# Performance work log

Hardware: AMD Instinct MI355X
Metric: run time of the kernel (lower is better)

The kernel has to match this reference:

```python
import jax, jax.numpy as jnp
import numpy as np

D_K = 256.0  # K_dim from __init__, used only as 1/sqrt(d_k) scale


def setup_inputs() -> dict:
    key = jax.random.key(0)
    ks = jax.random.split(key, 8)
    B, S, L, DQ, DK, DV, H = 8, 4096, 64, 1024, 1024, 1024, 256
    Q = jax.random.normal(ks[0], (B, S, DQ), dtype=jnp.float32)
    K = jax.random.normal(ks[1], (L, DK), dtype=jnp.float32)
    V = jax.random.normal(ks[2], (B, S, DV), dtype=jnp.float32)
    attn_mask = jax.random.randint(ks[3], (B, S, 1), 0, 2).astype(jnp.bool_)
    Wq_w = jax.random.normal(ks[4], (H, DQ), dtype=jnp.float32) * 0.02
    Wq_b = jnp.zeros((H,), dtype=jnp.float32)
    Wk_w = jax.random.normal(ks[5], (H, DK), dtype=jnp.float32) * 0.02
    Wk_b = jnp.zeros((H,), dtype=jnp.float32)
    return {"Q": Q, "K": K, "V": V, "attn_mask": attn_mask,
            "Wq_w": Wq_w, "Wq_b": Wq_b, "Wk_w": Wk_w, "Wk_b": Wk_b}


def reference(Q, K, V, attn_mask, Wq_w, Wq_b, Wk_w, Wk_b):
    # Projections (the original's expand/repeat + mul + sum is exactly a GEMM)
    kh = K @ Wk_w.T + Wk_b                                  # (L, 256)
    qh = (Q @ Wq_w.T + Wq_b) / jnp.sqrt(jnp.float32(D_K))   # (B, S, 256)
    # S[b,s,l] = sum_d qh[b,s,d]*kh[l,d]; scores sums over labels too
    S = jnp.einsum('bsd,ld->bsl', qh, kh)                   # (B, S, L)
    scores = S.sum(-1)[..., None] + attn_mask.astype(jnp.float32) * (-1e9)  # (B,S,1)
    scores = jnp.swapaxes(scores, -1, -2)                   # (B, 1, S)
    attn = jax.nn.softmax(scores, axis=-1)                  # (B, 1, S)
    context = jnp.matmul(attn, V)[:, 0, :]                  # (B, DV)
    return context, attn
```

## Files before the change

### kernel.cpp

```cpp
#include <hip/hip_runtime.h>
#include <hip/hip_bf16.h>
#include <cstddef>


#define B 8
#define S 4096
#define DQ 1024
#define H 256
#define L 64
#define RPB 16
#define NSC (S / RPB)

__global__ __launch_bounds__(256) void pre1_kernel(
        const float* __restrict__ K, const float* __restrict__ Wk_w,
        const float* __restrict__ Wk_b, float* __restrict__ ksum,
        float* __restrict__ denom) {
    __shared__ float sv[DQ];
    int t = threadIdx.x;
    if (blockIdx.x == 0 && t < B) denom[t] = 0.f;
    float4 a = {0.f, 0.f, 0.f, 0.f};
    const float* kp = K + t * 4;
#pragma unroll 8
    for (int l = 0; l < L; ++l) {
        float4 k = *(const float4*)(kp + (size_t)l * DQ);
        a.x += k.x; a.y += k.y; a.z += k.z; a.w += k.w;
    }
    *(float4*)(sv + t * 4) = a;
    __syncthreads();
    int wave = t >> 6, lane = t & 63;
    int d = blockIdx.x * 4 + wave;
    const float* wr = Wk_w + (size_t)d * DQ;
    float acc = 0.f;
#pragma unroll
    for (int j = 0; j < 4; ++j) {
        int idx = j * 256 + lane * 4;
        float4 x = *(const float4*)(wr + idx);
        float4 y = *(const float4*)(sv + idx);
        acc += x.x * y.x + x.y * y.y + x.z * y.z + x.w * y.w;
    }
    for (int off = 32; off; off >>= 1) acc += __shfl_down(acc, off);
    if (lane == 0) ksum[d] = acc + 64.f * Wk_b[d];
}

__global__ __launch_bounds__(256) void pre2_kernel(
        const float* __restrict__ Wq_w, const float* __restrict__ Wq_b,
        const float* __restrict__ ksum, float* __restrict__ w,
        float* __restrict__ bias) {
    __shared__ float ks[H];
    __shared__ float red[4][64];
    __shared__ float red2[4];
    ks[threadIdx.x] = ksum[threadIdx.x];
    __syncthreads();
    int wave = threadIdx.x >> 6, lane = threadIdx.x & 63;
    if (blockIdx.x < 16) {
        int c = blockIdx.x * 64 + lane;
        float acc = 0.f;
#pragma unroll 8
        for (int j = 0; j < 64; ++j) {
            int d = wave + 4 * j;
            acc += Wq_w[(size_t)d * DQ + c] * ks[d];
        }
        red[wave][lane] = acc;
        __syncthreads();
        if (wave == 0)
            w[c] = (red[0][lane] + red[1][lane] + red[2][lane] + red[3][lane]) * 0.0625f;
    } else {
        float v = Wq_b[threadIdx.x] * ks[threadIdx.x];
        for (int off = 32; off; off >>= 1) v += __shfl_down(v, off);
        if (lane == 0) red2[wave] = v;
        __syncthreads();
        if (threadIdx.x == 0)
            bias[0] = (red2[0] + red2[1] + red2[2] + red2[3]) * 0.0625f;
    }
}

__global__ __launch_bounds__(256) void fused_main_kernel(
        const float* __restrict__ Q, const float* __restrict__ V,
        const float* __restrict__ w, const float* __restrict__ bias,
        const int* __restrict__ mask,
        float* __restrict__ escore, float* __restrict__ denom,
        float* __restrict__ partial) {
    int sc = blockIdx.x, b = blockIdx.y, t = threadIdx.x;
    __shared__ float sp[RPB * 256];
    __shared__ float es[RPB];
    size_t rowbase = (size_t)b * S + (size_t)sc * RPB;

    const float* qb = Q + rowbase * DQ + t * 4;
    float4 wv = *(const float4*)(w + t * 4);
    float4 qv[RPB];
#pragma unroll
    for (int r = 0; r < RPB; ++r) qv[r] = *(const float4*)(qb + (size_t)r * DQ);
#pragma unroll
    for (int r = 0; r < RPB; ++r)
        sp[r * 256 + t] = qv[r].x * wv.x + qv[r].y * wv.y + qv[r].z * wv.z + qv[r].w * wv.w;
    __syncthreads();

    int r = t >> 4, j = t & 15;
    float s = 0.f;
#pragma unroll
    for (int k = 0; k < 16; ++k) s += sp[r * 256 + k * 16 + j];
    s += __shfl_xor(s, 8, 64);
    s += __shfl_xor(s, 4, 64);
    s += __shfl_xor(s, 2, 64);
    s += __shfl_xor(s, 1, 64);
    if (j == 0) {
        size_t row = rowbase + r;
        float e = mask[row] ? 0.f : __expf(s + bias[0]);
        es[r] = e;
        escore[row] = e;
    }
    __syncthreads();
    if (t == 0) {
        float d0 = 0.f;
#pragma unroll
        for (int k = 0; k < RPB; ++k) d0 += es[k];
        atomicAdd(denom + b, d0);
    }

    const float* vb = V + rowbase * DQ + t * 4;
    float4 acc = {0.f, 0.f, 0.f, 0.f};
#pragma unroll
    for (int s0 = 0; s0 < RPB; s0 += 8) {
        float4 v[8];
#pragma unroll
        for (int k = 0; k < 8; ++k) v[k] = *(const float4*)(vb + (size_t)(s0 + k) * DQ);
#pragma unroll
        for (int k = 0; k < 8; ++k) {
            float a = es[s0 + k];
            acc.x += a * v[k].x; acc.y += a * v[k].y;
            acc.z += a * v[k].z; acc.w += a * v[k].w;
        }
    }
    *(float4*)(partial + ((size_t)b * NSC + sc) * DQ + t * 4) = acc;
}

__global__ __launch_bounds__(256) void epilogue_kernel(
        const float* __restrict__ escore, const float* __restrict__ partial,
        const float* __restrict__ denom,
        float* __restrict__ ctx, float* __restrict__ attn) {
    if (blockIdx.x < 128) {
        int i = blockIdx.x * 256 + threadIdx.x;
        attn[i] = escore[i] / denom[i >> 12];
    } else {
        int idx = (blockIdx.x - 128) * 256 + threadIdx.x;
        int b = idx >> 10, d = idx & 1023;
        const float* p = partial + (size_t)b * NSC * DQ + d;
        float acc = 0.f;
#pragma unroll 8
        for (int sc = 0; sc < NSC; ++sc) acc += p[(size_t)sc * DQ];
        ctx[idx] = acc / denom[b];
    }
}

extern "C" void kernel_launch(void* const* d_in, const int* in_sizes, int n_in,
                              void* d_out, int out_size, void* d_ws, size_t ws_size,
                              hipStream_t stream) {
    const float* Q    = (const float*)d_in[0];
    const float* K    = (const float*)d_in[1];
    const float* V    = (const float*)d_in[2];
    const int*   mask = (const int*)d_in[3];
    const float* Wq_w = (const float*)d_in[4];
    const float* Wq_b = (const float*)d_in[5];
    const float* Wk_w = (const float*)d_in[6];
    const float* Wk_b = (const float*)d_in[7];

    float* ws     = (float*)d_ws;
    float* ksum   = ws;
    float* wv     = ws + 256;
    float* bias   = ws + 1280;
    float* denom  = ws + 1288;
    float* escore = ws + 4096;
    float* partial = ws + 4096 + B * S;

    float* ctx  = (float*)d_out;
    float* attn = (float*)d_out + B * DQ;

    pre1_kernel<<<H / 4, 256, 0, stream>>>(K, Wk_w, Wk_b, ksum, denom);
    pre2_kernel<<<17, 256, 0, stream>>>(Wq_w, Wq_b, ksum, wv, bias);
    fused_main_kernel<<<dim3(NSC, B), 256, 0, stream>>>(Q, V, wv, bias, mask,
                                                        escore, denom, partial);
    epilogue_kernel<<<160, 256, 0, stream>>>(escore, partial, denom, ctx, attn);
}
```

Baseline: 319.3 us.

## Split fused score/context kernel into separate scores and context kernels

The fused kernel that computed exp-scores from Q and then accumulated V within one block is split into two kernels. The scores kernel streams Q rows and writes exp-scores and denominators. The context kernel reads those scores and streams V with 32 rows per block, software-prefetching the next 8 rows, which halves the partial buffer the epilogue must reduce. The split adds a launch and a round-trip of the escore array, and loses the overlap of Q and V streaming inside one block.

```diff
diff --git a/kernel.cpp b/kernel.cpp
--- a/kernel.cpp
+++ b/kernel.cpp
@@ -8,8 +8,9 @@
 #define DQ 1024
 #define H 256
 #define L 64
-#define RPB 16
-#define NSC (S / RPB)
+#define SRPB 16
+#define CRPB 32
+#define NCHUNK (S / CRPB)
 
 __global__ __launch_bounds__(256) void pre1_kernel(
         const float* __restrict__ K, const float* __restrict__ Wk_w,
@@ -74,64 +75,89 @@
     }
 }
 
-__global__ __launch_bounds__(256) void fused_main_kernel(
-        const float* __restrict__ Q, const float* __restrict__ V,
-        const float* __restrict__ w, const float* __restrict__ bias,
-        const int* __restrict__ mask,
-        float* __restrict__ escore, float* __restrict__ denom,
-        float* __restrict__ partial) {
-    int sc = blockIdx.x, b = blockIdx.y, t = threadIdx.x;
-    __shared__ float sp[RPB * 256];
-    __shared__ float es[RPB];
-    size_t rowbase = (size_t)b * S + (size_t)sc * RPB;
-
+__global__ __launch_bounds__(256) void scores_kernel(
+        const float* __restrict__ Q, const float* __restrict__ w,
+        const float* __restrict__ bias, const int* __restrict__ mask,
+        float* __restrict__ escore, float* __restrict__ denom) {
+    int t = threadIdx.x, g = blockIdx.x;
+    __shared__ float sp[SRPB][264];
+    __shared__ float sp2[SRPB];
+    __shared__ int ml[SRPB];
+    size_t rowbase = (size_t)g * SRPB;
+    if (t < SRPB) ml[t] = mask[rowbase + t];
+    float sb = bias[0];
+    float4 wt = *(const float4*)(w + t * 4);
     const float* qb = Q + rowbase * DQ + t * 4;
-    float4 wv = *(const float4*)(w + t * 4);
-    float4 qv[RPB];
-#pragma unroll
-    for (int r = 0; r < RPB; ++r) qv[r] = *(const float4*)(qb + (size_t)r * DQ);
-#pragma unroll
-    for (int r = 0; r < RPB; ++r)
-        sp[r * 256 + t] = qv[r].x * wv.x + qv[r].y * wv.y + qv[r].z * wv.z + qv[r].w * wv.w;
+
+    float4 buf[8], buf2[8];
+#pragma unroll
+    for (int k = 0; k < 8; ++k) buf[k] = *(const float4*)(qb + (size_t)k * DQ);
+#pragma unroll
+    for (int k = 0; k < 8; ++k) buf2[k] = *(const float4*)(qb + (size_t)(8 + k) * DQ);
+    float acc[SRPB];
+#pragma unroll
+    for (int k = 0; k < 8; ++k)
+        acc[k] = buf[k].x * wt.x + buf[k].y * wt.y + buf[k].z * wt.z + buf[k].w * wt.w;
+#pragma unroll
+    for (int k = 0; k < 8; ++k)
+        acc[8 + k] = buf2[k].x * wt.x + buf2[k].y * wt.y + buf2[k].z * wt.z + buf2[k].w * wt.w;
+#pragma unroll
+    for (int r = 0; r < SRPB; ++r) sp[r][t] = acc[r];
     __syncthreads();
 
     int r = t >> 4, j = t & 15;
     float s = 0.f;
 #pragma unroll
-    for (int k = 0; k < 16; ++k) s += sp[r * 256 + k * 16 + j];
+    for (int k = 0; k < 16; ++k) s += sp[r][k * 16 + j];
     s += __shfl_xor(s, 8, 64);
     s += __shfl_xor(s, 4, 64);
     s += __shfl_xor(s, 2, 64);
     s += __shfl_xor(s, 1, 64);
     if (j == 0) {
-        size_t row = rowbase + r;
-        float e = mask[row] ? 0.f : __expf(s + bias[0]);
-        es[r] = e;
-        escore[row] = e;
+        float e = ml[r] ? 0.f : __expf(s + sb);
+        sp2[r] = e;
+        escore[rowbase + r] = e;
     }
     __syncthreads();
     if (t == 0) {
         float d0 = 0.f;
 #pragma unroll
-        for (int k = 0; k < RPB; ++k) d0 += es[k];
-        atomicAdd(denom + b, d0);
-    }
-
+        for (int k = 0; k < SRPB; ++k) d0 += sp2[k];
+        atomicAdd(denom + (g >> 8), d0);
+    }
+}
+
+__global__ __launch_bounds__(256) void ctx_kernel(
+        const float* __restrict__ V, const float* __restrict__ escore,
+        float* __restrict__ partial) {
+    int t = threadIdx.x, g = blockIdx.x;
+    __shared__ float es[CRPB];
+    size_t rowbase = (size_t)g * CRPB;
+    if (t < CRPB) es[t] = escore[rowbase + t];
+    __syncthreads();
     const float* vb = V + rowbase * DQ + t * 4;
     float4 acc = {0.f, 0.f, 0.f, 0.f};
-#pragma unroll
-    for (int s0 = 0; s0 < RPB; s0 += 8) {
-        float4 v[8];
-#pragma unroll
-        for (int k = 0; k < 8; ++k) v[k] = *(const float4*)(vb + (size_t)(s0 + k) * DQ);
+    float4 buf[8];
+#pragma unroll
+    for (int k = 0; k < 8; ++k) buf[k] = *(const float4*)(vb + (size_t)k * DQ);
+#pragma unroll
+    for (int rb = 0; rb < CRPB; rb += 8) {
+        float4 nbuf[8];
+        if (rb + 8 < CRPB) {
+#pragma unroll
+            for (int k = 0; k < 8; ++k)
+                nbuf[k] = *(const float4*)(vb + (size_t)(rb + 8 + k) * DQ);
+        }
 #pragma unroll
         for (int k = 0; k < 8; ++k) {
-            float a = es[s0 + k];
-            acc.x += a * v[k].x; acc.y += a * v[k].y;
-            acc.z += a * v[k].z; acc.w += a * v[k].w;
+            float a = es[rb + k];
+            acc.x += a * buf[k].x; acc.y += a * buf[k].y;
+            acc.z += a * buf[k].z; acc.w += a * buf[k].w;
         }
-    }
-    *(float4*)(partial + ((size_t)b * NSC + sc) * DQ + t * 4) = acc;
+#pragma unroll
+        for (int k = 0; k < 8; ++k) buf[k] = nbuf[k];
+    }
+    *(float4*)(partial + (size_t)g * DQ + t * 4) = acc;
 }
 
 __global__ __launch_bounds__(256) void epilogue_kernel(
@@ -144,10 +170,10 @@
     } else {
         int idx = (blockIdx.x - 128) * 256 + threadIdx.x;
         int b = idx >> 10, d = idx & 1023;
-        const float* p = partial + (size_t)b * NSC * DQ + d;
+        const float* p = partial + (size_t)b * NCHUNK * DQ + d;
         float acc = 0.f;
 #pragma unroll 8
-        for (int sc = 0; sc < NSC; ++sc) acc += p[(size_t)sc * DQ];
+        for (int k = 0; k < NCHUNK; ++k) acc += p[(size_t)k * DQ];
         ctx[idx] = acc / denom[b];
     }
 }
@@ -177,7 +203,7 @@
 
     pre1_kernel<<<H / 4, 256, 0, stream>>>(K, Wk_w, Wk_b, ksum, denom);
     pre2_kernel<<<17, 256, 0, stream>>>(Wq_w, Wq_b, ksum, wv, bias);
-    fused_main_kernel<<<dim3(NSC, B), 256, 0, stream>>>(Q, V, wv, bias, mask,
-                                                        escore, denom, partial);
+    scores_kernel<<<(B * S) / SRPB, 256, 0, stream>>>(Q, wv, bias, mask, escore, denom);
+    ctx_kernel<<<(B * S) / CRPB, 256, 0, stream>>>(V, escore, partial);
     epilogue_kernel<<<160, 256, 0, stream>>>(escore, partial, denom, ctx, attn);
 }
```

After: 313.5 us. Within noise of the previous version (-1.8%).
